# Kernel optimization log

Hardware: AMD Instinct MI355X
Metric: run time of the kernel (lower is better)

Reference implementation:

```python
import jax, jax.numpy as jnp
import numpy as np

NUM_GROUPS = 32
EPS = 1e-6


def group_norm(x, gamma, beta):
    # x: [b, c, n]
    b, c, n = x.shape
    xg = x.reshape(b, NUM_GROUPS, (c // NUM_GROUPS) * n)
    mean = xg.mean(axis=-1, keepdims=True)
    var = xg.var(axis=-1, keepdims=True)
    xg = (xg - mean) * jax.lax.rsqrt(var + EPS)
    x = xg.reshape(b, c, n)
    return x * gamma[None, :, None] + beta[None, :, None]


def conv1x1(x, w, bias):
    # x: [b, c, n], w: [out, in], bias: [out]
    return jnp.einsum('oc,bcn->bon', w, x) + bias[None, :, None]


def setup_inputs() -> dict:
    key = jax.random.key(0)
    ks = jax.random.split(key, 12)
    b, c, n = 16, 512, 2048
    scale = 1.0 / np.sqrt(c)
    inp = {
        'x': jax.random.normal(ks[0], (b, c, n), dtype=jnp.float32),
        'gn_gamma': jnp.ones((c,), dtype=jnp.float32),
        'gn_beta': jnp.zeros((c,), dtype=jnp.float32),
        'wq': jax.random.normal(ks[1], (c, c), dtype=jnp.float32) * scale,
        'bq': jnp.zeros((c,), dtype=jnp.float32),
        'wk': jax.random.normal(ks[2], (c, c), dtype=jnp.float32) * scale,
        'bk': jnp.zeros((c,), dtype=jnp.float32),
        'wv': jax.random.normal(ks[3], (c, c), dtype=jnp.float32) * scale,
        'bv': jnp.zeros((c,), dtype=jnp.float32),
        'wo': jax.random.normal(ks[4], (c, c), dtype=jnp.float32) * scale,
        'bo': jnp.zeros((c,), dtype=jnp.float32),
    }
    return inp


def reference(x, gn_gamma, gn_beta, wq, bq, wk, bk, wv, bv, wo, bo):
    # x: [b, c, n]
    c = x.shape[1]
    h = group_norm(x, gn_gamma, gn_beta)
    q = conv1x1(h, wq, bq)  # [b, c, n]
    k = conv1x1(h, wk, bk)  # [b, c, n]
    v = conv1x1(h, wv, bv)  # [b, c, n]
    # scores: q^T k  -> [b, n_q, n_kv]
    scores = jnp.einsum('bcn,bcm->bnm', q, k) * (c ** -0.5)
    attn = jax.nn.softmax(scores, axis=-1)  # softmax over keys (dim=2)
    # h = v @ attn^T  -> [b, c, n_q]
    out = jnp.einsum('bcm,bnm->bcn', v, attn)
    out = conv1x1(out, wo, bo)
    return x + out
```

## Files before the change

### kernel.cpp

```cpp
#include <hip/hip_runtime.h>
#include <hip/hip_bf16.h>
#include <math.h>

#define Bb 16
#define Cc 512
#define Nn 2048

typedef unsigned short u16;
typedef __attribute__((ext_vector_type(8))) short bf16x8;
typedef __attribute__((ext_vector_type(4))) float f32x4;

typedef __attribute__((address_space(3))) unsigned as3_u32;
typedef __attribute__((address_space(1))) const unsigned as1_u32;

__device__ __forceinline__ float b2f(u16 u){ unsigned x = ((unsigned)u) << 16; return __builtin_bit_cast(float, x); }
__device__ __forceinline__ u16 f2b(float f){
  unsigned x = __builtin_bit_cast(unsigned, f);
  x += 0x7fffu + ((x >> 16) & 1u);
  return (u16)(x >> 16);
}

__device__ __forceinline__ void gload16(const u16* g, u16* l){
  __builtin_amdgcn_global_load_lds((as1_u32*)(uintptr_t)(const void*)g,
                                   (as3_u32*)(uintptr_t)(void*)l, 16, 0, 0);
}

#define BAR() do{ __builtin_amdgcn_s_barrier(); asm volatile("" ::: "memory"); }while(0)
#define WAITV4() asm volatile("s_waitcnt vmcnt(4)" ::: "memory")
#define WAITV0() asm volatile("s_waitcnt vmcnt(0)" ::: "memory")

__global__ __launch_bounds__(256) void k_cvt(const float* __restrict__ s0, const float* __restrict__ s1,
                                             const float* __restrict__ s2,
                                             u16* __restrict__ d0, u16* __restrict__ d1, u16* __restrict__ d2){
  const float* s = (blockIdx.z == 0) ? s0 : (blockIdx.z == 1) ? s1 : s2;
  u16* d = (blockIdx.z == 0) ? d0 : (blockIdx.z == 1) ? d1 : d2;
  int i = blockIdx.x * 256 + threadIdx.x;
  float4 v = ((const float4*)s)[i];
  ushort4 o; o.x = f2b(v.x); o.y = f2b(v.y); o.z = f2b(v.z); o.w = f2b(v.w);
  ((ushort4*)d)[i] = o;
}

__global__ __launch_bounds__(256) void k_gn(const float* __restrict__ x,
                                            const float* __restrict__ gamma,
                                            const float* __restrict__ beta,
                                            u16* __restrict__ h){
  int bid = blockIdx.x;
  int b = bid >> 5, g = bid & 31;
  const float4* xv = (const float4*)(x + ((size_t)b * Cc + g * 16) * Nn);
  u16* hp = h + ((size_t)b * Cc + g * 16) * Nn;
  int t = threadIdx.x;
  float s = 0.f, ss = 0.f;
#pragma unroll 4
  for (int it = 0; it < 32; ++it){
    float4 v = xv[it * 256 + t];
    s  += v.x + v.y + v.z + v.w;
    ss += v.x * v.x + v.y * v.y + v.z * v.z + v.w * v.w;
  }
#pragma unroll
  for (int o = 32; o >= 1; o >>= 1){ s += __shfl_xor(s, o); ss += __shfl_xor(ss, o); }
  __shared__ float rs[4], rss[4];
  int w = t >> 6;
  if ((t & 63) == 0){ rs[w] = s; rss[w] = ss; }
  __syncthreads();
  s  = rs[0] + rs[1] + rs[2] + rs[3];
  ss = rss[0] + rss[1] + rss[2] + rss[3];
  float mean = s * (1.f / 32768.f);
  float var  = ss * (1.f / 32768.f) - mean * mean;
  float inv  = rsqrtf(var + 1e-6f);
#pragma unroll 4
  for (int it = 0; it < 32; ++it){
    int idx = it * 256 + t;
    float4 u = xv[idx];
    int ch = g * 16 + (idx >> 9);
    float ga = gamma[ch] * inv, be = beta[ch];
    ushort4 o;
    o.x = f2b((u.x - mean) * ga + be);
    o.y = f2b((u.y - mean) * ga + be);
    o.z = f2b((u.z - mean) * ga + be);
    o.w = f2b((u.w - mean) * ga + be);
    ((ushort4*)hp)[idx] = o;
  }
}

__global__ __launch_bounds__(256) void k_tr(const u16* __restrict__ h, u16* __restrict__ ht){
  __shared__ u16 lds[64 * 65];
  int b = blockIdx.z;
  int n0 = blockIdx.x * 64, c0 = blockIdx.y * 64;
  const u16* src = h + (size_t)b * Cc * Nn;
  u16* dst = ht + (size_t)b * Nn * Cc;
  int t = threadIdx.x;
  int jc = (t & 7) << 3;
  int r  = t >> 3;
#pragma unroll
  for (int it = 0; it < 2; ++it){
    int rr = r + it * 32;
    uint4 vv = *(const uint4*)(src + (size_t)(c0 + rr) * Nn + n0 + jc);
    u16* pv = (u16*)&vv;
#pragma unroll
    for (int e = 0; e < 8; ++e) lds[(jc + e) * 65 + rr] = pv[e];
  }
  __syncthreads();
#pragma unroll
  for (int it = 0; it < 2; ++it){
    int rn = r + it * 32;
    u16 tmp[8];
#pragma unroll
    for (int e = 0; e < 8; ++e) tmp[e] = lds[rn * 65 + jc + e];
    *(uint4*)(dst + (size_t)(n0 + rn) * Cc + c0 + jc) = *(const uint4*)tmp;
  }
}

#define SLOT_U16 16384

__device__ __forceinline__ void gemm256(const u16* __restrict__ A, int lda,
                                        const u16* __restrict__ B, int ldb, int K,
                                        u16* __restrict__ lds, f32x4 (&acc)[8][4]){
  const int tid = threadIdx.x;
  const int w = tid >> 6, lane = tid & 63;
  const int lr = lane & 15, lk = lane >> 4;
  const int wr = w >> 2, wc = w & 3;

  const int swzc = lk ^ ((lr >> 1) & 3);
  const int aoff = (wr * 128 + lr) * 32 + 8 * swzc;
  const int boff = 8192 + (wc * 64 + lr) * 32 + 8 * swzc;

  const int idx0 = w * 128 + lane;
  const int idx1 = idx0 + 64;
  const int r0s = idx0 >> 2, r1s = idx1 >> 2;
  const int c0 = (idx0 & 3) ^ ((r0s >> 1) & 3);
  const int c1 = (idx1 & 3) ^ ((r1s >> 1) & 3);
  const u16* gA0 = A + (size_t)r0s * lda + 8 * c0;
  const u16* gA1 = A + (size_t)r1s * lda + 8 * c1;
  const u16* gB0 = B + (size_t)r0s * ldb + 8 * c0;
  const u16* gB1 = B + (size_t)r1s * ldb + 8 * c1;
  const int dst0 = w * 1024;
  const int dst1 = dst0 + 512;

#pragma unroll
  for (int i = 0; i < 8; ++i)
#pragma unroll
    for (int j = 0; j < 4; ++j){ f32x4 z = {0.f,0.f,0.f,0.f}; acc[i][j] = z; }

  const int NT = K >> 5;

  gload16(gA0,      lds + dst0);            gload16(gA1,      lds + dst1);
  gload16(gB0,      lds + 8192 + dst0);     gload16(gB1,      lds + 8192 + dst1);
  gload16(gA0 + 32, lds + SLOT_U16 + dst0); gload16(gA1 + 32, lds + SLOT_U16 + dst1);
  gload16(gB0 + 32, lds + SLOT_U16 + 8192 + dst0);
  gload16(gB1 + 32, lds + SLOT_U16 + 8192 + dst1);
  WAITV4();
  BAR();

  int s = 0;
#pragma unroll 1
  for (int T = 0; T < NT; ++T){
    const u16* Asl = lds + s * SLOT_U16;
    int st = s + 2; if (st >= 3) st -= 3;
    u16* stl = lds + st * SLOT_U16;
    const bool pf = (T + 2) < NT;
    const int kk = (T + 2) << 5;

    bf16x8 a0[4], b0[4];
#pragma unroll
    for (int i = 0; i < 4; ++i) a0[i] = *(const bf16x8*)(Asl + aoff + i * 512);
#pragma unroll
    for (int j = 0; j < 4; ++j) b0[j] = *(const bf16x8*)(Asl + boff + j * 512);
    if (pf){ gload16(gA0 + kk, stl + dst0); gload16(gA1 + kk, stl + dst1); }
    BAR();
    __builtin_amdgcn_s_setprio(1);
#pragma unroll
    for (int i = 0; i < 4; ++i)
#pragma unroll
      for (int j = 0; j < 4; ++j)
        acc[i][j] = __builtin_amdgcn_mfma_f32_16x16x32_bf16(a0[i], b0[j], acc[i][j], 0, 0, 0);
    __builtin_amdgcn_s_setprio(0);
    BAR();

    bf16x8 a1[4];
#pragma unroll
    for (int i = 0; i < 4; ++i) a1[i] = *(const bf16x8*)(Asl + aoff + (i + 4) * 512);
    if (pf){ gload16(gB0 + kk, stl + 8192 + dst0); gload16(gB1 + kk, stl + 8192 + dst1); }
    BAR();
    __builtin_amdgcn_s_setprio(1);
#pragma unroll
    for (int i = 0; i < 4; ++i)
#pragma unroll
      for (int j = 0; j < 4; ++j)
        acc[i + 4][j] = __builtin_amdgcn_mfma_f32_16x16x32_bf16(a1[i], b0[j], acc[i + 4][j], 0, 0, 0);
    __builtin_amdgcn_s_setprio(0);
    if (pf){ WAITV4(); } else { WAITV0(); }
    BAR();
    s = (s + 1 == 3) ? 0 : s + 1;
  }
}

#define EPI_COORDS \
  int lane = threadIdx.x & 63, w = threadIdx.x >> 6; \
  int wr = w >> 2, wc = w & 3; \
  int lr = lane & 15; \
  int r0 = (lane >> 4) << 2;

__global__ __launch_bounds__(512, 2) void k_qkt(const u16* __restrict__ ht,
                                                const u16* __restrict__ wqb, const u16* __restrict__ wkb,
                                                const float* __restrict__ bq, const float* __restrict__ bk,
                                                u16* __restrict__ qt, u16* __restrict__ kt){
  __shared__ u16 lds[3 * SLOT_U16];
  int z = blockIdx.z, b = z >> 1, p = z & 1;
  int m0 = blockIdx.x * 256, n0 = blockIdx.y * 256;
  const u16* A = ht + (size_t)b * Nn * Cc + (size_t)m0 * Cc;
  const u16* B = (p ? wkb : wqb) + (size_t)n0 * Cc;
  const float* bias = p ? bk : bq;
  u16* out = (p ? kt : qt) + (size_t)b * Nn * Cc;
  f32x4 acc[8][4];
  gemm256(A, Cc, B, Cc, Cc, lds, acc);
  EPI_COORDS
#pragma unroll
  for (int i = 0; i < 8; ++i)
#pragma unroll
    for (int j = 0; j < 4; ++j){
      int col = n0 + wc * 64 + j * 16 + lr;
      float bi = bias[col];
      int row = m0 + wr * 128 + i * 16 + r0;
#pragma unroll
      for (int r = 0; r < 4; ++r)
        out[(size_t)(row + r) * Cc + col] = f2b(acc[i][j][r] + bi);
    }
}

__global__ __launch_bounds__(512, 2) void k_vproj(const u16* __restrict__ wvb, const u16* __restrict__ ht,
                                                  const float* __restrict__ bv, u16* __restrict__ v){
  __shared__ u16 lds[3 * SLOT_U16];
  int b = blockIdx.z;
  int m0 = blockIdx.x * 256, n0 = blockIdx.y * 256;
  const u16* A = wvb + (size_t)m0 * Cc;
  const u16* B = ht + (size_t)b * Nn * Cc + (size_t)n0 * Cc;
  u16* out = v + (size_t)b * Cc * Nn;
  f32x4 acc[8][4];
  gemm256(A, Cc, B, Cc, Cc, lds, acc);
  EPI_COORDS
#pragma unroll
  for (int i = 0; i < 8; ++i)
#pragma unroll
    for (int j = 0; j < 4; ++j){
      int col = n0 + wc * 64 + j * 16 + lr;
      int row = m0 + wr * 128 + i * 16 + r0;
#pragma unroll
      for (int r = 0; r < 4; ++r)
        out[(size_t)(row + r) * Nn + col] = f2b(acc[i][j][r] + bv[row + r]);
    }
}

__global__ __launch_bounds__(512, 2) void k_scores(const u16* __restrict__ qt, const u16* __restrict__ kt,
                                                   u16* __restrict__ p){
  __shared__ u16 lds[3 * SLOT_U16];
  int b = blockIdx.z;
  int m0 = blockIdx.x * 256, n0 = blockIdx.y * 256;
  const u16* A = qt + (size_t)b * Nn * Cc + (size_t)m0 * Cc;
  const u16* B = kt + (size_t)b * Nn * Cc + (size_t)n0 * Cc;
  u16* pb = p + (size_t)b * Nn * Nn;
  f32x4 acc[8][4];
  gemm256(A, Cc, B, Cc, Cc, lds, acc);
  const float scale = 0.044194173824159216f;
  EPI_COORDS
#pragma unroll
  for (int i = 0; i < 8; ++i)
#pragma unroll
    for (int j = 0; j < 4; ++j){
      int col = n0 + wc * 64 + j * 16 + lr;
      int row = m0 + wr * 128 + i * 16 + r0;
#pragma unroll
      for (int r = 0; r < 4; ++r)
        pb[(size_t)(row + r) * Nn + col] = f2b(acc[i][j][r] * scale);
    }
}

__global__ __launch_bounds__(256) void k_softmax(u16* __restrict__ p){
  size_t r = blockIdx.x;
  u16* row = p + r * (size_t)Nn;
  int t = threadIdx.x;
  uint4 raw = ((uint4*)row)[t];
  u16* u = (u16*)&raw;
  float vals[8];
  float m = -1e30f;
#pragma unroll
  for (int e = 0; e < 8; ++e){ vals[e] = b2f(u[e]); m = fmaxf(m, vals[e]); }
#pragma unroll
  for (int o = 32; o >= 1; o >>= 1) m = fmaxf(m, __shfl_xor(m, o));
  __shared__ float sm[4], ssum[4];
  int w = t >> 6;
  if ((t & 63) == 0) sm[w] = m;
  __syncthreads();
  m = fmaxf(fmaxf(sm[0], sm[1]), fmaxf(sm[2], sm[3]));
  float s = 0.f;
#pragma unroll
  for (int e = 0; e < 8; ++e){ vals[e] = __expf(vals[e] - m); s += vals[e]; }
#pragma unroll
  for (int o = 32; o >= 1; o >>= 1) s += __shfl_xor(s, o);
  if ((t & 63) == 0) ssum[w] = s;
  __syncthreads();
  s = ssum[0] + ssum[1] + ssum[2] + ssum[3];
  float inv = 1.f / s;
#pragma unroll
  for (int e = 0; e < 8; ++e) u[e] = f2b(vals[e] * inv);
  ((uint4*)row)[t] = raw;
}

__global__ __launch_bounds__(512, 2) void k_pv(const u16* __restrict__ p, const u16* __restrict__ v,
                                               u16* __restrict__ aot){
  __shared__ u16 lds[3 * SLOT_U16];
  int b = blockIdx.z;
  int m0 = blockIdx.x * 256, n0 = blockIdx.y * 256;
  const u16* A = p + (size_t)b * Nn * Nn + (size_t)m0 * Nn;
  const u16* B = v + (size_t)b * Cc * Nn + (size_t)n0 * Nn;
  u16* out = aot + (size_t)b * Nn * Cc;
  f32x4 acc[8][4];
  gemm256(A, Nn, B, Nn, Nn, lds, acc);
  EPI_COORDS
#pragma unroll
  for (int i = 0; i < 8; ++i)
#pragma unroll
    for (int j = 0; j < 4; ++j){
      int col = n0 + wc * 64 + j * 16 + lr;
      int row = m0 + wr * 128 + i * 16 + r0;
#pragma unroll
      for (int r = 0; r < 4; ++r)
        out[(size_t)(row + r) * Cc + col] = f2b(acc[i][j][r]);
    }
}

__global__ __launch_bounds__(512, 2) void k_proj(const u16* __restrict__ wob, const u16* __restrict__ aot,
                                                 const float* __restrict__ bo, const float* __restrict__ x,
                                                 float* __restrict__ out){
  __shared__ u16 lds[3 * SLOT_U16];
  int b = blockIdx.z;
  int m0 = blockIdx.x * 256, n0 = blockIdx.y * 256;
  const u16* A = wob + (size_t)m0 * Cc;
  const u16* B = aot + (size_t)b * Nn * Cc + (size_t)n0 * Cc;
  f32x4 acc[8][4];
  gemm256(A, Cc, B, Cc, Cc, lds, acc);
  size_t base = (size_t)b * Cc * Nn;
  EPI_COORDS
#pragma unroll
  for (int i = 0; i < 8; ++i)
#pragma unroll
    for (int j = 0; j < 4; ++j){
      int col = n0 + wc * 64 + j * 16 + lr;
      int row = m0 + wr * 128 + i * 16 + r0;
#pragma unroll
      for (int r = 0; r < 4; ++r){
        size_t idx = base + (size_t)(row + r) * Nn + col;
        out[idx] = x[idx] + bo[row + r] + acc[i][j][r];
      }
    }
}

extern "C" void kernel_launch(void* const* d_in, const int* in_sizes, int n_in,
                              void* d_out, int out_size, void* d_ws, size_t ws_size,
                              hipStream_t stream){
  const float* x     = (const float*)d_in[0];
  const float* gamma = (const float*)d_in[1];
  const float* beta  = (const float*)d_in[2];
  const float* wq = (const float*)d_in[3];
  const float* bq = (const float*)d_in[4];
  const float* wk = (const float*)d_in[5];
  const float* bk = (const float*)d_in[6];
  const float* wv = (const float*)d_in[7];
  const float* bv = (const float*)d_in[8];
  const float* wo = (const float*)d_in[9];
  const float* bo = (const float*)d_in[10];
  float* out = (float*)d_out;

  char* ws = (char*)d_ws;
  const size_t MB = 1048576ull;
  u16* ht  = (u16*)(ws);
  u16* qt  = (u16*)(ws + 32 * MB);
  u16* kt  = (u16*)(ws + 64 * MB);
  u16* v   = (u16*)(ws + 96 * MB);
  u16* P   = (u16*)(ws + 128 * MB);
  u16* wqb = P;
  u16* wkb = P + 262144;
  u16* wvb = P + 524288;
  u16* h   = (u16*)(ws + 130 * MB);
  u16* wob = qt;
  u16* aot = ht;

  k_cvt<<<dim3(256, 1, 3), 256, 0, stream>>>(wq, wk, wv, wqb, wkb, wvb);
  k_gn<<<dim3(512), 256, 0, stream>>>(x, gamma, beta, h);
  k_tr<<<dim3(32, 8, 16), 256, 0, stream>>>(h, ht);
  k_qkt<<<dim3(8, 2, 32), 512, 0, stream>>>(ht, wqb, wkb, bq, bk, qt, kt);
  k_vproj<<<dim3(2, 8, 16), 512, 0, stream>>>(wvb, ht, bv, v);
  k_scores<<<dim3(8, 8, 16), 512, 0, stream>>>(qt, kt, P);
  k_cvt<<<dim3(256, 1, 1), 256, 0, stream>>>(wo, wo, wo, wob, wob, wob);
  k_softmax<<<dim3(32768), 256, 0, stream>>>(P);
  k_pv<<<dim3(8, 2, 16), 512, 0, stream>>>(P, v, aot);
  k_proj<<<dim3(2, 8, 16), 512, 0, stream>>>(wob, aot, bo, x, out);
}
```

Baseline: 365.6 us.

## Deepen GEMM LDS pipeline to four stages, vectorize epilogues, swizzle block order

The shared GEMM mainloop moves from a three-slot LDS ring with split A/B prefetch and two MFMA phases to a four-slot ring. It prefetches three tiles ahead, does all 32 MFMAs per K-step with one barrier, and swaps the MFMA operands so each lane holds four consecutive output columns. The epilogues then write vectorized ushort4/float4 stores instead of scattered scalar stores. The scores and PV kernels also remap a 1D grid with an XCD-style swizzle for cache locality. Costs are more LDS per block, which may affect occupancy at two blocks per CU, and more live registers.

```diff
diff --git a/kernel.cpp b/kernel.cpp
--- a/kernel.cpp
+++ b/kernel.cpp
@@ -26,6 +26,7 @@
 }
 
 #define BAR() do{ __builtin_amdgcn_s_barrier(); asm volatile("" ::: "memory"); }while(0)
+#define WAITV8() asm volatile("s_waitcnt vmcnt(8)" ::: "memory")
 #define WAITV4() asm volatile("s_waitcnt vmcnt(4)" ::: "memory")
 #define WAITV0() asm volatile("s_waitcnt vmcnt(0)" ::: "memory")
 
@@ -143,54 +144,45 @@
 
   const int NT = K >> 5;
 
-  gload16(gA0,      lds + dst0);            gload16(gA1,      lds + dst1);
-  gload16(gB0,      lds + 8192 + dst0);     gload16(gB1,      lds + 8192 + dst1);
-  gload16(gA0 + 32, lds + SLOT_U16 + dst0); gload16(gA1 + 32, lds + SLOT_U16 + dst1);
-  gload16(gB0 + 32, lds + SLOT_U16 + 8192 + dst0);
-  gload16(gB1 + 32, lds + SLOT_U16 + 8192 + dst1);
-  WAITV4();
+#pragma unroll
+  for (int t = 0; t < 3; ++t){
+    u16* sl = lds + t * SLOT_U16;
+    const int kk = t << 5;
+    gload16(gA0 + kk, sl + dst0);        gload16(gA1 + kk, sl + dst1);
+    gload16(gB0 + kk, sl + 8192 + dst0); gload16(gB1 + kk, sl + 8192 + dst1);
+  }
+  WAITV8();
   BAR();
 
-  int s = 0;
 #pragma unroll 1
   for (int T = 0; T < NT; ++T){
-    const u16* Asl = lds + s * SLOT_U16;
-    int st = s + 2; if (st >= 3) st -= 3;
-    u16* stl = lds + st * SLOT_U16;
-    const bool pf = (T + 2) < NT;
-    const int kk = (T + 2) << 5;
-
-    bf16x8 a0[4], b0[4];
-#pragma unroll
-    for (int i = 0; i < 4; ++i) a0[i] = *(const bf16x8*)(Asl + aoff + i * 512);
-#pragma unroll
-    for (int j = 0; j < 4; ++j) b0[j] = *(const bf16x8*)(Asl + boff + j * 512);
-    if (pf){ gload16(gA0 + kk, stl + dst0); gload16(gA1 + kk, stl + dst1); }
+    const u16* Asl = lds + (T & 3) * SLOT_U16;
+
+    if (T + 3 < NT){
+      u16* stl = lds + ((T + 3) & 3) * SLOT_U16;
+      const int kk = (T + 3) << 5;
+      gload16(gA0 + kk, stl + dst0);        gload16(gA1 + kk, stl + dst1);
+      gload16(gB0 + kk, stl + 8192 + dst0); gload16(gB1 + kk, stl + 8192 + dst1);
+    }
+
+    bf16x8 a[8], b[4];
+#pragma unroll
+    for (int i = 0; i < 8; ++i) a[i] = *(const bf16x8*)(Asl + aoff + i * 512);
+#pragma unroll
+    for (int j = 0; j < 4; ++j) b[j] = *(const bf16x8*)(Asl + boff + j * 512);
+
+    __builtin_amdgcn_s_setprio(1);
+#pragma unroll
+    for (int i = 0; i < 8; ++i)
+#pragma unroll
+      for (int j = 0; j < 4; ++j)
+        acc[i][j] = __builtin_amdgcn_mfma_f32_16x16x32_bf16(b[j], a[i], acc[i][j], 0, 0, 0);
+    __builtin_amdgcn_s_setprio(0);
+
+    if (T + 3 < NT)      { WAITV8(); }
+    else if (T + 2 < NT) { WAITV4(); }
+    else if (T + 1 < NT) { WAITV0(); }
     BAR();
-    __builtin_amdgcn_s_setprio(1);
-#pragma unroll
-    for (int i = 0; i < 4; ++i)
-#pragma unroll
-      for (int j = 0; j < 4; ++j)
-        acc[i][j] = __builtin_amdgcn_mfma_f32_16x16x32_bf16(a0[i], b0[j], acc[i][j], 0, 0, 0);
-    __builtin_amdgcn_s_setprio(0);
-    BAR();
-
-    bf16x8 a1[4];
-#pragma unroll
-    for (int i = 0; i < 4; ++i) a1[i] = *(const bf16x8*)(Asl + aoff + (i + 4) * 512);
-    if (pf){ gload16(gB0 + kk, stl + 8192 + dst0); gload16(gB1 + kk, stl + 8192 + dst1); }
-    BAR();
-    __builtin_amdgcn_s_setprio(1);
-#pragma unroll
-    for (int i = 0; i < 4; ++i)
-#pragma unroll
-      for (int j = 0; j < 4; ++j)
-        acc[i + 4][j] = __builtin_amdgcn_mfma_f32_16x16x32_bf16(a1[i], b0[j], acc[i + 4][j], 0, 0, 0);
-    __builtin_amdgcn_s_setprio(0);
-    if (pf){ WAITV4(); } else { WAITV0(); }
-    BAR();
-    s = (s + 1 == 3) ? 0 : s + 1;
   }
 }
 
@@ -198,13 +190,13 @@
   int lane = threadIdx.x & 63, w = threadIdx.x >> 6; \
   int wr = w >> 2, wc = w & 3; \
   int lr = lane & 15; \
-  int r0 = (lane >> 4) << 2;
+  int g4 = (lane >> 4) << 2;
 
 __global__ __launch_bounds__(512, 2) void k_qkt(const u16* __restrict__ ht,
                                                 const u16* __restrict__ wqb, const u16* __restrict__ wkb,
                                                 const float* __restrict__ bq, const float* __restrict__ bk,
                                                 u16* __restrict__ qt, u16* __restrict__ kt){
-  __shared__ u16 lds[3 * SLOT_U16];
+  __shared__ u16 lds[4 * SLOT_U16];
   int z = blockIdx.z, b = z >> 1, p = z & 1;
   int m0 = blockIdx.x * 256, n0 = blockIdx.y * 256;
   const u16* A = ht + (size_t)b * Nn * Cc + (size_t)m0 * Cc;
@@ -215,21 +207,25 @@
   gemm256(A, Cc, B, Cc, Cc, lds, acc);
   EPI_COORDS
 #pragma unroll
-  for (int i = 0; i < 8; ++i)
+  for (int i = 0; i < 8; ++i){
+    int row = m0 + wr * 128 + i * 16 + lr;
 #pragma unroll
     for (int j = 0; j < 4; ++j){
-      int col = n0 + wc * 64 + j * 16 + lr;
-      float bi = bias[col];
-      int row = m0 + wr * 128 + i * 16 + r0;
-#pragma unroll
-      for (int r = 0; r < 4; ++r)
-        out[(size_t)(row + r) * Cc + col] = f2b(acc[i][j][r] + bi);
-    }
+      int coln = n0 + wc * 64 + j * 16 + g4;
+      float4 bi = *(const float4*)(bias + coln);
+      ushort4 o;
+      o.x = f2b(acc[i][j][0] + bi.x);
+      o.y = f2b(acc[i][j][1] + bi.y);
+      o.z = f2b(acc[i][j][2] + bi.z);
+      o.w = f2b(acc[i][j][3] + bi.w);
+      *(ushort4*)(out + (size_t)row * Cc + coln) = o;
+    }
+  }
 }
 
 __global__ __launch_bounds__(512, 2) void k_vproj(const u16* __restrict__ wvb, const u16* __restrict__ ht,
                                                   const float* __restrict__ bv, u16* __restrict__ v){
-  __shared__ u16 lds[3 * SLOT_U16];
+  __shared__ u16 lds[4 * SLOT_U16];
   int b = blockIdx.z;
   int m0 = blockIdx.x * 256, n0 = blockIdx.y * 256;
   const u16* A = wvb + (size_t)m0 * Cc;
@@ -239,22 +235,29 @@
   gemm256(A, Cc, B, Cc, Cc, lds, acc);
   EPI_COORDS
 #pragma unroll
-  for (int i = 0; i < 8; ++i)
+  for (int i = 0; i < 8; ++i){
+    int row = m0 + wr * 128 + i * 16 + lr;
+    float bi = bv[row];
 #pragma unroll
     for (int j = 0; j < 4; ++j){
-      int col = n0 + wc * 64 + j * 16 + lr;
-      int row = m0 + wr * 128 + i * 16 + r0;
-#pragma unroll
-      for (int r = 0; r < 4; ++r)
-        out[(size_t)(row + r) * Nn + col] = f2b(acc[i][j][r] + bv[row + r]);
-    }
+      int coln = n0 + wc * 64 + j * 16 + g4;
+      ushort4 o;
+      o.x = f2b(acc[i][j][0] + bi);
+      o.y = f2b(acc[i][j][1] + bi);
+      o.z = f2b(acc[i][j][2] + bi);
+      o.w = f2b(acc[i][j][3] + bi);
+      *(ushort4*)(out + (size_t)row * Nn + coln) = o;
+    }
+  }
 }
 
 __global__ __launch_bounds__(512, 2) void k_scores(const u16* __restrict__ qt, const u16* __restrict__ kt,
                                                    u16* __restrict__ p){
-  __shared__ u16 lds[3 * SLOT_U16];
-  int b = blockIdx.z;
-  int m0 = blockIdx.x * 256, n0 = blockIdx.y * 256;
+  __shared__ u16 lds[4 * SLOT_U16];
+  int bid = blockIdx.x;
+  int swz = (bid & 7) * 128 + (bid >> 3);
+  int b = swz >> 6, rem = swz & 63;
+  int m0 = (rem & 7) * 256, n0 = (rem >> 3) * 256;
   const u16* A = qt + (size_t)b * Nn * Cc + (size_t)m0 * Cc;
   const u16* B = kt + (size_t)b * Nn * Cc + (size_t)n0 * Cc;
   u16* pb = p + (size_t)b * Nn * Nn;
@@ -263,15 +266,19 @@
   const float scale = 0.044194173824159216f;
   EPI_COORDS
 #pragma unroll
-  for (int i = 0; i < 8; ++i)
+  for (int i = 0; i < 8; ++i){
+    int row = m0 + wr * 128 + i * 16 + lr;
 #pragma unroll
     for (int j = 0; j < 4; ++j){
-      int col = n0 + wc * 64 + j * 16 + lr;
-      int row = m0 + wr * 128 + i * 16 + r0;
-#pragma unroll
-      for (int r = 0; r < 4; ++r)
-        pb[(size_t)(row + r) * Nn + col] = f2b(acc[i][j][r] * scale);
-    }
+      int coln = n0 + wc * 64 + j * 16 + g4;
+      ushort4 o;
+      o.x = f2b(acc[i][j][0] * scale);
+      o.y = f2b(acc[i][j][1] * scale);
+      o.z = f2b(acc[i][j][2] * scale);
+      o.w = f2b(acc[i][j][3] * scale);
+      *(ushort4*)(pb + (size_t)row * Nn + coln) = o;
+    }
+  }
 }
 
 __global__ __launch_bounds__(256) void k_softmax(u16* __restrict__ p){
@@ -307,9 +314,11 @@
 
 __global__ __launch_bounds__(512, 2) void k_pv(const u16* __restrict__ p, const u16* __restrict__ v,
                                                u16* __restrict__ aot){
-  __shared__ u16 lds[3 * SLOT_U16];
-  int b = blockIdx.z;
-  int m0 = blockIdx.x * 256, n0 = blockIdx.y * 256;
+  __shared__ u16 lds[4 * SLOT_U16];
+  int bid = blockIdx.x;
+  int swz = (bid & 7) * 32 + (bid >> 3);
+  int b = swz >> 4, rem = swz & 15;
+  int m0 = (rem & 7) * 256, n0 = (rem >> 3) * 256;
   const u16* A = p + (size_t)b * Nn * Nn + (size_t)m0 * Nn;
   const u16* B = v + (size_t)b * Cc * Nn + (size_t)n0 * Nn;
   u16* out = aot + (size_t)b * Nn * Cc;
@@ -317,21 +326,25 @@
   gemm256(A, Nn, B, Nn, Nn, lds, acc);
   EPI_COORDS
 #pragma unroll
-  for (int i = 0; i < 8; ++i)
+  for (int i = 0; i < 8; ++i){
+    int row = m0 + wr * 128 + i * 16 + lr;
 #pragma unroll
     for (int j = 0; j < 4; ++j){
-      int col = n0 + wc * 64 + j * 16 + lr;
-      int row = m0 + wr * 128 + i * 16 + r0;
-#pragma unroll
-      for (int r = 0; r < 4; ++r)
-        out[(size_t)(row + r) * Cc + col] = f2b(acc[i][j][r]);
-    }
+      int coln = n0 + wc * 64 + j * 16 + g4;
+      ushort4 o;
+      o.x = f2b(acc[i][j][0]);
+      o.y = f2b(acc[i][j][1]);
+      o.z = f2b(acc[i][j][2]);
+      o.w = f2b(acc[i][j][3]);
+      *(ushort4*)(out + (size_t)row * Cc + coln) = o;
+    }
+  }
 }
 
 __global__ __launch_bounds__(512, 2) void k_proj(const u16* __restrict__ wob, const u16* __restrict__ aot,
                                                  const float* __restrict__ bo, const float* __restrict__ x,
                                                  float* __restrict__ out){
-  __shared__ u16 lds[3 * SLOT_U16];
+  __shared__ u16 lds[4 * SLOT_U16];
   int b = blockIdx.z;
   int m0 = blockIdx.x * 256, n0 = blockIdx.y * 256;
   const u16* A = wob + (size_t)m0 * Cc;
@@ -341,17 +354,22 @@
   size_t base = (size_t)b * Cc * Nn;
   EPI_COORDS
 #pragma unroll
-  for (int i = 0; i < 8; ++i)
+  for (int i = 0; i < 8; ++i){
+    int row = m0 + wr * 128 + i * 16 + lr;
+    float bi = bo[row];
 #pragma unroll
     for (int j = 0; j < 4; ++j){
-      int col = n0 + wc * 64 + j * 16 + lr;
-      int row = m0 + wr * 128 + i * 16 + r0;
-#pragma unroll
-      for (int r = 0; r < 4; ++r){
-        size_t idx = base + (size_t)(row + r) * Nn + col;
-        out[idx] = x[idx] + bo[row + r] + acc[i][j][r];
-      }
-    }
+      int coln = n0 + wc * 64 + j * 16 + g4;
+      size_t idx = base + (size_t)row * Nn + coln;
+      float4 xv = *(const float4*)(x + idx);
+      float4 o;
+      o.x = xv.x + bi + acc[i][j][0];
+      o.y = xv.y + bi + acc[i][j][1];
+      o.z = xv.z + bi + acc[i][j][2];
+      o.w = xv.w + bi + acc[i][j][3];
+      *(float4*)(out + idx) = o;
+    }
+  }
 }
 
 extern "C" void kernel_launch(void* const* d_in, const int* in_sizes, int n_in,
@@ -389,9 +407,9 @@
   k_tr<<<dim3(32, 8, 16), 256, 0, stream>>>(h, ht);
   k_qkt<<<dim3(8, 2, 32), 512, 0, stream>>>(ht, wqb, wkb, bq, bk, qt, kt);
   k_vproj<<<dim3(2, 8, 16), 512, 0, stream>>>(wvb, ht, bv, v);
-  k_scores<<<dim3(8, 8, 16), 512, 0, stream>>>(qt, kt, P);
+  k_scores<<<dim3(1024), 512, 0, stream>>>(qt, kt, P);
   k_cvt<<<dim3(256, 1, 1), 256, 0, stream>>>(wo, wo, wo, wob, wob, wob);
   k_softmax<<<dim3(32768), 256, 0, stream>>>(P);
-  k_pv<<<dim3(8, 2, 16), 512, 0, stream>>>(P, v, aot);
+  k_pv<<<dim3(256), 512, 0, stream>>>(P, v, aot);
   k_proj<<<dim3(2, 8, 16), 512, 0, stream>>>(wob, aot, bo, x, out);
 }
```

After: 386.0 us. 5.6% more time.

## Fuse scores, softmax and PV into a single flash-style attention kernel

Applied to the files above, without the earlier changes.

Replaces the separate scores GEMM, row softmax and P·V GEMM with one kernel that keeps each 128-query tile's scores on chip. Per 128-key block it computes QK^T with MFMA, exponentiates into an LDS tile and accumulates P·V. It divides by the running row sum only at the end. This avoids writing, rereading and rewriting the 2048x2048 bf16 probability matrix per batch. In exchange it skips max subtraction before exp, so large scores could overflow. It also runs with one 512-thread block per CU and synchronises after every small K/V chunk. The wo conversion moves to its own scratch slot at the start.

```diff
diff --git a/kernel.cpp b/kernel.cpp
--- a/kernel.cpp
+++ b/kernel.cpp
@@ -110,7 +110,7 @@
   }
 }
 
-#define SLOT_U16 16384
+#define GSLOT 16384
 
 __device__ __forceinline__ void gemm256(const u16* __restrict__ A, int lda,
                                         const u16* __restrict__ B, int ldb, int K,
@@ -145,18 +145,18 @@
 
   gload16(gA0,      lds + dst0);            gload16(gA1,      lds + dst1);
   gload16(gB0,      lds + 8192 + dst0);     gload16(gB1,      lds + 8192 + dst1);
-  gload16(gA0 + 32, lds + SLOT_U16 + dst0); gload16(gA1 + 32, lds + SLOT_U16 + dst1);
-  gload16(gB0 + 32, lds + SLOT_U16 + 8192 + dst0);
-  gload16(gB1 + 32, lds + SLOT_U16 + 8192 + dst1);
+  gload16(gA0 + 32, lds + GSLOT + dst0);    gload16(gA1 + 32, lds + GSLOT + dst1);
+  gload16(gB0 + 32, lds + GSLOT + 8192 + dst0);
+  gload16(gB1 + 32, lds + GSLOT + 8192 + dst1);
   WAITV4();
   BAR();
 
   int s = 0;
 #pragma unroll 1
   for (int T = 0; T < NT; ++T){
-    const u16* Asl = lds + s * SLOT_U16;
+    const u16* Asl = lds + s * GSLOT;
     int st = s + 2; if (st >= 3) st -= 3;
-    u16* stl = lds + st * SLOT_U16;
+    u16* stl = lds + st * GSLOT;
     const bool pf = (T + 2) < NT;
     const int kk = (T + 2) << 5;
 
@@ -204,7 +204,7 @@
                                                 const u16* __restrict__ wqb, const u16* __restrict__ wkb,
                                                 const float* __restrict__ bq, const float* __restrict__ bk,
                                                 u16* __restrict__ qt, u16* __restrict__ kt){
-  __shared__ u16 lds[3 * SLOT_U16];
+  __shared__ u16 lds[3 * GSLOT];
   int z = blockIdx.z, b = z >> 1, p = z & 1;
   int m0 = blockIdx.x * 256, n0 = blockIdx.y * 256;
   const u16* A = ht + (size_t)b * Nn * Cc + (size_t)m0 * Cc;
@@ -229,7 +229,7 @@
 
 __global__ __launch_bounds__(512, 2) void k_vproj(const u16* __restrict__ wvb, const u16* __restrict__ ht,
                                                   const float* __restrict__ bv, u16* __restrict__ v){
-  __shared__ u16 lds[3 * SLOT_U16];
+  __shared__ u16 lds[3 * GSLOT];
   int b = blockIdx.z;
   int m0 = blockIdx.x * 256, n0 = blockIdx.y * 256;
   const u16* A = wvb + (size_t)m0 * Cc;
@@ -250,88 +250,150 @@
     }
 }
 
-__global__ __launch_bounds__(512, 2) void k_scores(const u16* __restrict__ qt, const u16* __restrict__ kt,
-                                                   u16* __restrict__ p){
-  __shared__ u16 lds[3 * SLOT_U16];
-  int b = blockIdx.z;
-  int m0 = blockIdx.x * 256, n0 = blockIdx.y * 256;
-  const u16* A = qt + (size_t)b * Nn * Cc + (size_t)m0 * Cc;
-  const u16* B = kt + (size_t)b * Nn * Cc + (size_t)n0 * Cc;
-  u16* pb = p + (size_t)b * Nn * Nn;
-  f32x4 acc[8][4];
-  gemm256(A, Cc, B, Cc, Cc, lds, acc);
+__global__ __launch_bounds__(512, 1) void k_attn(const u16* __restrict__ qt,
+                                                 const u16* __restrict__ kt,
+                                                 const u16* __restrict__ vv,
+                                                 u16* __restrict__ aot){
+  __shared__ u16 qk[2 * 16384];
+  __shared__ u16 vl[2 * 8192];
+  __shared__ u16 pl[16384];
+
+  const int bid = blockIdx.x;
+  const int xcd = bid & 7, sb = bid >> 3;
+  const int b = (xcd << 1) | (sb >> 4);
+  const int qtile = sb & 15;
+  const u16* Qb = qt + (size_t)b * Nn * Cc + (size_t)qtile * 128 * Cc;
+  const u16* Kb = kt + (size_t)b * Nn * Cc;
+  const u16* Vb = vv + (size_t)b * Cc * Nn;
+  u16* outp = aot + (size_t)b * Nn * Cc + (size_t)qtile * 128 * Cc;
+
+  const int tid = threadIdx.x;
+  const int w = tid >> 6, lane = tid & 63;
+  const int lr = lane & 15, lk = lane >> 4;
+  const int g4 = lk << 2;
+
+  const int srow = tid >> 2;
+  const int csw = (tid & 3) ^ ((tid >> 3) & 3);
+  const size_t qks_off = (size_t)srow * Cc + 8 * csw;
+  const size_t vs_off  = (size_t)srow * Nn + 8 * csw;
+  const int ldst = tid * 8;
+
+  const int qrow = w * 16 + lr;
+  const int qoff = qrow * 32 + 8 * (lk ^ ((qrow >> 1) & 3));
+  int rfoff[8];
+#pragma unroll
+  for (int j = 0; j < 8; ++j){
+    int r = j * 16 + lr;
+    rfoff[j] = r * 32 + 8 * (lk ^ ((r >> 1) & 3));
+  }
+  const int pbase = w * 2048 + lr * 128;
+  const int phalf = (lk & 1) * 4;
+  const int ph2 = lk >> 1;
+
+  f32x4 accO[4][8];
+#pragma unroll
+  for (int a = 0; a < 4; ++a)
+#pragma unroll
+    for (int c = 0; c < 8; ++c){ f32x4 z = {0.f,0.f,0.f,0.f}; accO[a][c] = z; }
+  float lsum = 0.f;
   const float scale = 0.044194173824159216f;
-  EPI_COORDS
-#pragma unroll
-  for (int i = 0; i < 8; ++i)
-#pragma unroll
-    for (int j = 0; j < 4; ++j){
-      int col = n0 + wc * 64 + j * 16 + lr;
-      int row = m0 + wr * 128 + i * 16 + r0;
-#pragma unroll
-      for (int r = 0; r < 4; ++r)
-        pb[(size_t)(row + r) * Nn + col] = f2b(acc[i][j][r] * scale);
-    }
-}
-
-__global__ __launch_bounds__(256) void k_softmax(u16* __restrict__ p){
-  size_t r = blockIdx.x;
-  u16* row = p + r * (size_t)Nn;
-  int t = threadIdx.x;
-  uint4 raw = ((uint4*)row)[t];
-  u16* u = (u16*)&raw;
-  float vals[8];
-  float m = -1e30f;
-#pragma unroll
-  for (int e = 0; e < 8; ++e){ vals[e] = b2f(u[e]); m = fmaxf(m, vals[e]); }
-#pragma unroll
-  for (int o = 32; o >= 1; o >>= 1) m = fmaxf(m, __shfl_xor(m, o));
-  __shared__ float sm[4], ssum[4];
-  int w = t >> 6;
-  if ((t & 63) == 0) sm[w] = m;
-  __syncthreads();
-  m = fmaxf(fmaxf(sm[0], sm[1]), fmaxf(sm[2], sm[3]));
-  float s = 0.f;
-#pragma unroll
-  for (int e = 0; e < 8; ++e){ vals[e] = __expf(vals[e] - m); s += vals[e]; }
-#pragma unroll
-  for (int o = 32; o >= 1; o >>= 1) s += __shfl_xor(s, o);
-  if ((t & 63) == 0) ssum[w] = s;
-  __syncthreads();
-  s = ssum[0] + ssum[1] + ssum[2] + ssum[3];
-  float inv = 1.f / s;
-#pragma unroll
-  for (int e = 0; e < 8; ++e) u[e] = f2b(vals[e] * inv);
-  ((uint4*)row)[t] = raw;
-}
-
-__global__ __launch_bounds__(512, 2) void k_pv(const u16* __restrict__ p, const u16* __restrict__ v,
-                                               u16* __restrict__ aot){
-  __shared__ u16 lds[3 * SLOT_U16];
-  int b = blockIdx.z;
-  int m0 = blockIdx.x * 256, n0 = blockIdx.y * 256;
-  const u16* A = p + (size_t)b * Nn * Nn + (size_t)m0 * Nn;
-  const u16* B = v + (size_t)b * Cc * Nn + (size_t)n0 * Nn;
-  u16* out = aot + (size_t)b * Nn * Cc;
-  f32x4 acc[8][4];
-  gemm256(A, Nn, B, Nn, Nn, lds, acc);
-  EPI_COORDS
-#pragma unroll
-  for (int i = 0; i < 8; ++i)
-#pragma unroll
-    for (int j = 0; j < 4; ++j){
-      int col = n0 + wc * 64 + j * 16 + lr;
-      int row = m0 + wr * 128 + i * 16 + r0;
-#pragma unroll
-      for (int r = 0; r < 4; ++r)
-        out[(size_t)(row + r) * Cc + col] = f2b(acc[i][j][r]);
+
+#pragma unroll 1
+  for (int t = 0; t < 16; ++t){
+    const u16* Kt = Kb + (size_t)t * 128 * Cc;
+    const int kv0 = t * 128;
+
+    f32x4 acc2[8];
+#pragma unroll
+    for (int j = 0; j < 8; ++j){ f32x4 z = {0.f,0.f,0.f,0.f}; acc2[j] = z; }
+
+#define STQK(sl, kb) do{ \
+      gload16(Qb + qks_off + (kb),      qk + (sl) * 16384 + ldst); \
+      gload16(Kt + qks_off + (kb),      qk + (sl) * 16384 + 4096 + ldst); \
+      gload16(Qb + qks_off + (kb) + 32, qk + (sl) * 16384 + 8192 + ldst); \
+      gload16(Kt + qks_off + (kb) + 32, qk + (sl) * 16384 + 12288 + ldst); }while(0)
+
+    STQK(0, 0);
+    WAITV0(); BAR();
+#pragma unroll 1
+    for (int ch = 0; ch < 8; ++ch){
+      const u16* cs = qk + (ch & 1) * 16384;
+      if (ch < 7) STQK((ch & 1) ^ 1, (ch + 1) * 64);
+#pragma unroll
+      for (int ks2 = 0; ks2 < 2; ++ks2){
+        bf16x8 qf = *(const bf16x8*)(cs + ks2 * 8192 + qoff);
+#pragma unroll
+        for (int j = 0; j < 8; ++j){
+          bf16x8 kf = *(const bf16x8*)(cs + ks2 * 8192 + 4096 + rfoff[j]);
+          acc2[j] = __builtin_amdgcn_mfma_f32_16x16x32_bf16(kf, qf, acc2[j], 0, 0, 0);
+        }
+      }
+      if (ch < 7) WAITV0();
+      BAR();
+    }
+
+#pragma unroll
+    for (int j = 0; j < 8; ++j){
+      float e0 = __expf(acc2[j][0] * scale);
+      float e1 = __expf(acc2[j][1] * scale);
+      float e2 = __expf(acc2[j][2] * scale);
+      float e3 = __expf(acc2[j][3] * scale);
+      lsum += (e0 + e1) + (e2 + e3);
+      ushort4 pk; pk.x = f2b(e0); pk.y = f2b(e1); pk.z = f2b(e2); pk.w = f2b(e3);
+      int swz8 = (2 * j + ph2) ^ lr;
+      *(ushort4*)(pl + pbase + swz8 * 8 + phalf) = pk;
+    }
+
+#define STV(sl, cc, kvh) do{ \
+      const u16* vp = Vb + (size_t)(cc) * 128 * Nn + kv0 + (kvh) * 64 + vs_off; \
+      gload16(vp,      vl + (sl) * 8192 + ldst); \
+      gload16(vp + 32, vl + (sl) * 8192 + 4096 + ldst); }while(0)
+
+    STV(0, 0, 0);
+    WAITV0(); BAR();
+#pragma unroll 1
+    for (int pc = 0; pc < 8; ++pc){
+      const int cc = pc >> 1, kvh = pc & 1;
+      const u16* vs = vl + (pc & 1) * 8192;
+      if (pc < 7) STV((pc & 1) ^ 1, (pc + 1) >> 1, (pc + 1) & 1);
+#pragma unroll
+      for (int ks2 = 0; ks2 < 2; ++ks2){
+        const int ksg = kvh * 2 + ks2;
+        bf16x8 pf = *(const bf16x8*)(pl + pbase + ((ksg * 4 + lk) ^ lr) * 8);
+#pragma unroll
+        for (int ci = 0; ci < 8; ++ci){
+          bf16x8 vf = *(const bf16x8*)(vs + ks2 * 4096 + rfoff[ci]);
+          accO[cc][ci] = __builtin_amdgcn_mfma_f32_16x16x32_bf16(vf, pf, accO[cc][ci], 0, 0, 0);
+        }
+      }
+      if (pc < 7) WAITV0();
+      BAR();
+    }
+#undef STQK
+#undef STV
+  }
+
+  lsum += __shfl_xor(lsum, 16);
+  lsum += __shfl_xor(lsum, 32);
+  float inv = 1.f / lsum;
+#pragma unroll
+  for (int cc = 0; cc < 4; ++cc)
+#pragma unroll
+    for (int ci = 0; ci < 8; ++ci){
+      int col = cc * 128 + ci * 16 + g4;
+      ushort4 o;
+      o.x = f2b(accO[cc][ci][0] * inv);
+      o.y = f2b(accO[cc][ci][1] * inv);
+      o.z = f2b(accO[cc][ci][2] * inv);
+      o.w = f2b(accO[cc][ci][3] * inv);
+      *(ushort4*)(outp + (size_t)(w * 16 + lr) * Cc + col) = o;
     }
 }
 
 __global__ __launch_bounds__(512, 2) void k_proj(const u16* __restrict__ wob, const u16* __restrict__ aot,
                                                  const float* __restrict__ bo, const float* __restrict__ x,
                                                  float* __restrict__ out){
-  __shared__ u16 lds[3 * SLOT_U16];
+  __shared__ u16 lds[3 * GSLOT];
   int b = blockIdx.z;
   int m0 = blockIdx.x * 256, n0 = blockIdx.y * 256;
   const u16* A = wob + (size_t)m0 * Cc;
@@ -376,22 +438,20 @@
   u16* qt  = (u16*)(ws + 32 * MB);
   u16* kt  = (u16*)(ws + 64 * MB);
   u16* v   = (u16*)(ws + 96 * MB);
-  u16* P   = (u16*)(ws + 128 * MB);
-  u16* wqb = P;
-  u16* wkb = P + 262144;
-  u16* wvb = P + 524288;
+  u16* scr = (u16*)(ws + 128 * MB);
+  u16* wqb = scr;
+  u16* wkb = scr + 262144;
+  u16* wvb = scr + 524288;
+  u16* wob = scr + 786432;
   u16* h   = (u16*)(ws + 130 * MB);
-  u16* wob = qt;
   u16* aot = ht;
 
   k_cvt<<<dim3(256, 1, 3), 256, 0, stream>>>(wq, wk, wv, wqb, wkb, wvb);
+  k_cvt<<<dim3(256, 1, 1), 256, 0, stream>>>(wo, wo, wo, wob, wob, wob);
   k_gn<<<dim3(512), 256, 0, stream>>>(x, gamma, beta, h);
   k_tr<<<dim3(32, 8, 16), 256, 0, stream>>>(h, ht);
   k_qkt<<<dim3(8, 2, 32), 512, 0, stream>>>(ht, wqb, wkb, bq, bk, qt, kt);
   k_vproj<<<dim3(2, 8, 16), 512, 0, stream>>>(wvb, ht, bv, v);
-  k_scores<<<dim3(8, 8, 16), 512, 0, stream>>>(qt, kt, P);
-  k_cvt<<<dim3(256, 1, 1), 256, 0, stream>>>(wo, wo, wo, wob, wob, wob);
-  k_softmax<<<dim3(32768), 256, 0, stream>>>(P);
-  k_pv<<<dim3(8, 2, 16), 512, 0, stream>>>(P, v, aot);
+  k_attn<<<dim3(256), 512, 0, stream>>>(qt, kt, v, aot);
   k_proj<<<dim3(2, 8, 16), 512, 0, stream>>>(wob, aot, bo, x, out);
 }
```

New measurement: 957.8 us. 2.62x slower.
